# Kernel optimization log

Measured on AMD Instinct MI355X. Metric: run time of the kernel, lower is better.

The kernel has to match this reference:

```python
import jax, jax.numpy as jnp
import numpy as np
import math

B, S, HID = 1, 2048, 2048
H, KVH, HD = 16, 4, 128
LEVEL = 256


def _rope_tables(seq_len, dim, dtype=jnp.float32):
    inv_freq = 1.0 / (10000.0 ** (np.arange(0, dim, 2, dtype=np.float32) / dim))
    ang = np.arange(seq_len, dtype=np.float32)[:, None] * inv_freq[None, :]  # [S, HD/2]
    emb = np.concatenate([ang, ang], axis=-1)  # [S, HD]
    return jnp.asarray(np.cos(emb), dtype)[None], jnp.asarray(np.sin(emb), dtype)[None]


def setup_inputs() -> dict:
    key = jax.random.key(0)
    ks = jax.random.split(key, 6)
    hidden_states = jax.random.normal(ks[0], (B, S, HID), jnp.float32)
    w_std = 1.0 / math.sqrt(HID)
    Wq = jax.random.normal(ks[1], (H * HD, HID), jnp.float32) * w_std
    Wk = jax.random.normal(ks[2], (KVH * HD, HID), jnp.float32) * w_std
    Wv = jax.random.normal(ks[3], (KVH * HD, HID), jnp.float32) * w_std
    Wo = jax.random.normal(ks[4], (HID, H * HD), jnp.float32) * w_std
    cos, sin = _rope_tables(S, HD)
    # additive causal mask [1,1,S,S]
    tri = jnp.tril(jnp.ones((S, S), jnp.bool_))
    attention_mask = jnp.where(tri, 0.0, -1e9).astype(jnp.float32)[None, None]
    return {
        "hidden_states": hidden_states,
        "Wq": Wq, "Wk": Wk, "Wv": Wv, "Wo": Wo,
        "s_q": jnp.full((1,), 0.05, jnp.float32),
        "s_k": jnp.full((1,), 0.05, jnp.float32),
        "s_v": jnp.full((1,), 0.05, jnp.float32),
        "s_attn": jnp.full((1,), 0.004, jnp.float32),
        "s_out": jnp.full((1,), 0.02, jnp.float32),
        "cos": cos, "sin": sin,
        "attention_mask": attention_mask,
    }


def _lsq(x, s, level, sym):
    # LSQ fake-quant: learned per-tensor step s, STE round, LSQ grad-scale on s.
    if sym:
        qn, qp = -level // 2, level // 2 - 1
    else:
        qn, qp = 0, level - 1
    g = 1.0 / math.sqrt(x.size * qp)          # LSQ gradient scale (static)
    s = jnp.abs(s)
    s_eff = s * g + jax.lax.stop_gradient(s - s * g)  # fwd = s, bwd grad *= g
    v = jnp.clip(x / s_eff, qn, qp)
    q = v + jax.lax.stop_gradient(jnp.round(v) - v)   # STE round
    return q * s_eff


def _rotate_half(x):
    x1, x2 = jnp.split(x, 2, axis=-1)
    return jnp.concatenate([-x2, x1], axis=-1)


def _attn_fwd(hidden_states, Wq, Wk, Wv, Wo, s_q, s_k, s_v, s_attn, s_out,
              cos, sin, attention_mask):
    b, s_len, _ = hidden_states.shape
    # projections -> [B, heads, S, HD]
    q = (hidden_states @ Wq.T).reshape(b, s_len, H, HD).transpose(0, 2, 1, 3)
    q = _lsq(q, s_q, LEVEL, sym=True)
    k = (hidden_states @ Wk.T).reshape(b, s_len, KVH, HD).transpose(0, 2, 1, 3)
    k = _lsq(k, s_k, LEVEL, sym=True)
    v = (hidden_states @ Wv.T).reshape(b, s_len, KVH, HD).transpose(0, 2, 1, 3)
    v = _lsq(v, s_v, LEVEL, sym=True)
    # RoPE (after quant, matching source order)
    c, si = cos[:, None], sin[:, None]  # [B,1,S,HD]
    q = q * c + _rotate_half(q) * si
    k = k * c + _rotate_half(k) * si
    # GQA repeat
    groups = H // KVH
    k = jnp.repeat(k, groups, axis=1)
    v = jnp.repeat(v, groups, axis=1)
    scores = jnp.einsum("bhqd,bhkd->bhqk", q, k) / math.sqrt(HD)
    scores = scores + attention_mask[:, :, :, :s_len]
    attn = jax.nn.softmax(scores.astype(jnp.float32), axis=-1).astype(q.dtype)
    attn = _lsq(attn, s_attn, LEVEL, sym=False)
    out = jnp.einsum("bhqk,bhkd->bhqd", attn, v)
    out = _lsq(out, s_out, LEVEL, sym=False)
    out = out.transpose(0, 2, 1, 3).reshape(b, s_len, H * HD)
    out = out @ Wo.T
    return out, attn


def reference(hidden_states, Wq, Wk, Wv, Wo, s_q, s_k, s_v, s_attn, s_out,
              cos, sin, attention_mask):
    return _attn_fwd(hidden_states, Wq, Wk, Wv, Wo, s_q, s_k, s_v, s_attn,
                     s_out, cos, sin, attention_mask)
```

## Files before the change

kernel.cpp:

```cpp
#include <hip/hip_runtime.h>
#include <math.h>

#define S_LEN 2048
#define HID_DIM 2048
#define NH 16
#define NKVH 4
#define HD 128
#define QD (NH*HD)
#define KD (NKVH*HD)
#define NQKV 3072

typedef _Float16 half8_t __attribute__((ext_vector_type(8)));
typedef _Float16 half4_t __attribute__((ext_vector_type(4)));
typedef float f32x4 __attribute__((ext_vector_type(4)));

#define BM 128
#define BN 128
#define BK 32

typedef const __attribute__((address_space(1))) char gas_char;
typedef __attribute__((address_space(3))) char las_char;
#define GL16(gp, lp) __builtin_amdgcn_global_load_lds((gas_char*)(gp), (las_char*)(lp), 16, 0, 0)

template<int LA, int LB, bool AF32, bool PSM>
__global__ __launch_bounds__(256)
void gemm_f16(const void* __restrict__ Ap, const _Float16* __restrict__ Alo,
              int lda, long long strA,
              const _Float16* __restrict__ Bhi, const _Float16* __restrict__ Blo,
              int ldb, long long strB, int divB,
              void* __restrict__ Cp, int ldc, long long strC,
              int K, float scale_c, const float* sc1, const float* sc2,
              const float* preAp,
              int qmode, const float* q1, const float* q2, const float* q3,
              int causal, int triK, float* __restrict__ pml)
{
    int bz = blockIdx.z;
    int m0 = blockIdx.y * BM, n0 = blockIdx.x * BN;
    if (causal && n0 > m0 + (BM - 1)) return;
    int Keff = K;
    if (triK && (m0 + BM) < Keff) Keff = m0 + BM;

    const _Float16* Ahi = AF32 ? nullptr : (const _Float16*)Ap + bz * strA;
    const _Float16* AloP = (LA == 2) ? Alo + bz * strA : nullptr;
    const float* Af = AF32 ? (const float*)Ap + bz * strA : nullptr;
    const _Float16* BhiP = Bhi + (long long)(bz / divB) * strB;
    const _Float16* BloP = (LB == 2) ? Blo + (long long)(bz / divB) * strB : nullptr;
    float* Cf = (float*)Cp + bz * strC;
    _Float16* Ch = (_Float16*)Cp + bz * strC;

    float preA = 1.f;
    if (AF32) preA = 1.f / fabsf(preAp[0]);

    __shared__ _Float16 lds[(LA + LB) * 4096];
    _Float16* As0 = lds;
    _Float16* As1 = lds + 4096;
    _Float16* Bs0 = lds + LA * 4096;
    _Float16* Bs1 = lds + (LA + 1) * 4096;

    int t = threadIdx.x;
    int srow = t >> 2;
    int gsw = (srow >> 1) & 3;
    int gc = ((t & 3) ^ gsw) * 8;
    int w = t >> 6, lane = t & 63;
    int wm = (w >> 1) * 64, wn = (w & 1) * 64;
    int lr = lane & 15, lg = lane >> 4;
    int fco = ((lg ^ ((lr >> 1) & 3))) * 8;

    f32x4 acc[4][4];
    #pragma unroll
    for (int i = 0; i < 4; ++i)
        #pragma unroll
        for (int j = 0; j < 4; ++j)
            acc[i][j] = (f32x4){0.f, 0.f, 0.f, 0.f};

    for (int k0 = 0; k0 < Keff; k0 += BK) {
        f32x4 aF[2][2];
        if constexpr (AF32) {
            #pragma unroll
            for (int rep = 0; rep < 2; ++rep) {
                long long ai = (long long)(m0 + rep * 64 + srow) * lda + k0 + gc;
                aF[rep][0] = *(const f32x4*)&Af[ai];
                aF[rep][1] = *(const f32x4*)&Af[ai + 4];
            }
        }
        __syncthreads();
        #pragma unroll
        for (int rep = 0; rep < 2; ++rep) {
            int row = rep * 64 + srow;
            int lo = rep * 2048 + t * 8;
            if constexpr (!AF32) {
                long long ai = (long long)(m0 + row) * lda + k0 + gc;
                GL16(Ahi + ai, As0 + lo);
                if constexpr (LA == 2) GL16(AloP + ai, As1 + lo);
            }
            long long bi = (long long)(n0 + row) * ldb + k0 + gc;
            GL16(BhiP + bi, Bs0 + lo);
            if constexpr (LB == 2) GL16(BloP + bi, Bs1 + lo);
        }
        if constexpr (AF32) {
            #pragma unroll
            for (int rep = 0; rep < 2; ++rep) {
                half8_t h;
                #pragma unroll
                for (int e = 0; e < 4; ++e) {
                    h[e]     = (_Float16)(aF[rep][0][e] * preA);
                    h[e + 4] = (_Float16)(aF[rep][1][e] * preA);
                }
                *(half8_t*)&As0[rep * 2048 + t * 8] = h;
            }
        }
        __syncthreads();

        half8_t a0[4], b0[4];
        #pragma unroll
        for (int i = 0; i < 4; ++i) a0[i] = *(const half8_t*)&As0[(wm + i*16 + lr) * 32 + fco];
        #pragma unroll
        for (int j = 0; j < 4; ++j) b0[j] = *(const half8_t*)&Bs0[(wn + j*16 + lr) * 32 + fco];
        #pragma unroll
        for (int i = 0; i < 4; ++i)
            #pragma unroll
            for (int j = 0; j < 4; ++j)
                acc[i][j] = __builtin_amdgcn_mfma_f32_16x16x32_f16(a0[i], b0[j], acc[i][j], 0, 0, 0);
        if constexpr (LB == 2) {
            half8_t b1[4];
            #pragma unroll
            for (int j = 0; j < 4; ++j) b1[j] = *(const half8_t*)&Bs1[(wn + j*16 + lr) * 32 + fco];
            #pragma unroll
            for (int i = 0; i < 4; ++i)
                #pragma unroll
                for (int j = 0; j < 4; ++j)
                    acc[i][j] = __builtin_amdgcn_mfma_f32_16x16x32_f16(a0[i], b1[j], acc[i][j], 0, 0, 0);
        }
        if constexpr (LA == 2) {
            half8_t a1[4];
            #pragma unroll
            for (int i = 0; i < 4; ++i) a1[i] = *(const half8_t*)&As1[(wm + i*16 + lr) * 32 + fco];
            #pragma unroll
            for (int i = 0; i < 4; ++i)
                #pragma unroll
                for (int j = 0; j < 4; ++j)
                    acc[i][j] = __builtin_amdgcn_mfma_f32_16x16x32_f16(a1[i], b0[j], acc[i][j], 0, 0, 0);
        }
    }

    float se = scale_c;
    if (sc1) se *= fabsf(sc1[0]);
    if (sc2) se *= fabsf(sc2[0]);
    float sv = 1.f;
    if (qmode == 3) {
        const float* sp = (n0 < 2048) ? q1 : ((n0 < 2560) ? q2 : q3);
        sv = fabsf(sp[0]);
        qmode = 1;
    } else if (qmode) {
        sv = fabsf(q1[0]);
    }

    #pragma unroll
    for (int i = 0; i < 4; ++i)
        #pragma unroll
        for (int j = 0; j < 4; ++j)
            #pragma unroll
            for (int r = 0; r < 4; ++r) {
                long long row = m0 + wm + i * 16 + lg * 4 + r;
                long long col = n0 + wn + j * 16 + lr;
                float v = acc[i][j][r] * se;
                if (qmode == 0) {
                    Cf[row * (long long)ldc + col] = v;
                } else if (qmode == 1) {
                    float u = rintf(fminf(fmaxf(v / sv, -128.f), 127.f));
                    Ch[row * (long long)ldc + col] = (_Float16)u;
                } else {
                    float u = rintf(fminf(fmaxf(v / sv, 0.f), 255.f));
                    Ch[row * (long long)ldc + col] = (_Float16)u;
                }
            }

    if constexpr (PSM) {
        int cb64 = (n0 + wn) >> 6;
        #pragma unroll
        for (int i = 0; i < 4; ++i)
            #pragma unroll
            for (int r = 0; r < 4; ++r) {
                int row = m0 + wm + i * 16 + lg * 4 + r;
                float vv[4];
                float mloc = -INFINITY;
                #pragma unroll
                for (int j = 0; j < 4; ++j) {
                    int col = n0 + wn + j * 16 + lr;
                    float v = acc[i][j][r] * se;
                    vv[j] = (col <= row) ? v : -INFINITY;
                    mloc = fmaxf(mloc, vv[j]);
                }
                #pragma unroll
                for (int o = 1; o < 16; o <<= 1) mloc = fmaxf(mloc, __shfl_xor(mloc, o));
                float sloc = 0.f;
                #pragma unroll
                for (int j = 0; j < 4; ++j) sloc += expf(vv[j] - mloc);
                #pragma unroll
                for (int o = 1; o < 16; o <<= 1) sloc += __shfl_xor(sloc, o);
                if (lr == 0) {
                    long long idx = (((long long)bz * S_LEN + row) * 32 + cb64) * 2;
                    pml[idx] = mloc;
                    pml[idx + 1] = sloc;
                }
            }
    }
}

__global__ __launch_bounds__(256)
void reduce_ml(const float* __restrict__ pml, float* __restrict__ fml)
{
    int id = blockIdx.x * 256 + threadIdx.x;
    int r = id & (S_LEN - 1);
    int nb = (r >> 6) + 1;
    float m = -INFINITY, l = 0.f;
    const float* p = pml + (long long)id * 64;
    for (int cb = 0; cb < nb; ++cb) {
        float mp = p[cb * 2], lp = p[cb * 2 + 1];
        float mn = fmaxf(m, mp);
        l = l * expf(m - mn) + lp * expf(mp - mn);
        m = mn;
    }
    fml[id * 2] = m;
    fml[id * 2 + 1] = l;
}

__global__ __launch_bounds__(256)
void fused_pv(float* __restrict__ attn, const _Float16* __restrict__ vT,
              const float* __restrict__ fml, _Float16* __restrict__ ao,
              const float* s_at_p, const float* s_v_p, const float* s_out_p)
{
    int rb = blockIdx.x;
    int h = blockIdx.y;
    int m0 = rb * 64;
    float* S = attn + (long long)h * S_LEN * S_LEN;
    const _Float16* V = vT + (long long)(h >> 2) * HD * S_LEN;

    float sa = fabsf(s_at_p[0]);
    float seo = sa * fabsf(s_v_p[0]) / fabsf(s_out_p[0]);

    __shared__ _Float16 Bs[128 * 32];
    __shared__ float ml[64][2];

    int t = threadIdx.x;
    int w = t >> 6, lane = t & 63;
    int lr = lane & 15, lg = lane >> 4;
    int wr0 = m0 + w * 16;
    int row = wr0 + lr;

    if (t < 64) {
        ml[t][0] = fml[((long long)h * S_LEN + m0 + t) * 2];
        ml[t][1] = fml[((long long)h * S_LEN + m0 + t) * 2 + 1];
    }
    __syncthreads();
    float mrow = ml[w * 16 + lr][0];
    float lrow = ml[w * 16 + lr][1];

    int srow = t >> 2;
    int gsw = (srow >> 1) & 3;
    int gc = ((t & 3) ^ gsw) * 8;
    int fco = ((lg ^ ((lr >> 1) & 3))) * 8;

    f32x4 acc[8];
    #pragma unroll
    for (int j = 0; j < 8; ++j) acc[j] = (f32x4){0.f, 0.f, 0.f, 0.f};

    int kmax = m0 + 64;
    for (int k0 = 0; k0 < kmax; k0 += 32) {
        __syncthreads();
        #pragma unroll
        for (int rep = 0; rep < 2; ++rep)
            GL16(&V[(long long)(rep * 64 + srow) * S_LEN + k0 + gc], &Bs[rep * 2048 + t * 8]);

        int c0 = k0 + lg * 8;
        long long sbase = (long long)row * S_LEN + c0;
        f32x4 s1 = *(const f32x4*)&S[sbase];
        f32x4 s2 = *(const f32x4*)&S[sbase + 4];
        half8_t af;
        f32x4 o1, o2;
        #pragma unroll
        for (int e = 0; e < 8; ++e) {
            float sv_ = (e < 4) ? s1[e] : s2[e - 4];
            float u = 0.f;
            if (c0 + e <= row) {
                float p = expf(sv_ - mrow) / lrow;
                u = rintf(fminf(fmaxf(p / sa, 0.f), 255.f));
            }
            af[e] = (_Float16)u;
            if (e < 4) o1[e] = u * sa; else o2[e - 4] = u * sa;
        }
        *(f32x4*)&S[sbase] = o1;
        *(f32x4*)&S[sbase + 4] = o2;

        __syncthreads();
        if (k0 <= wr0 + 15) {
            half8_t bf[8];
            #pragma unroll
            for (int j = 0; j < 8; ++j)
                bf[j] = *(const half8_t*)&Bs[(j * 16 + lr) * 32 + fco];
            #pragma unroll
            for (int j = 0; j < 8; ++j)
                acc[j] = __builtin_amdgcn_mfma_f32_16x16x32_f16(af, bf[j], acc[j], 0, 0, 0);
        }
    }

    {
        int rr = t >> 2, l4 = (t & 3) * 4;
        f32x4 z = (f32x4){0.f, 0.f, 0.f, 0.f};
        for (int cc = kmax + l4; cc < S_LEN; cc += 16)
            *(f32x4*)&S[(long long)(m0 + rr) * S_LEN + cc] = z;
    }

    #pragma unroll
    for (int j = 0; j < 8; ++j)
        #pragma unroll
        for (int r = 0; r < 4; ++r) {
            int orow = wr0 + lg * 4 + r;
            int d = j * 16 + lr;
            float u = rintf(fminf(fmaxf(acc[j][r] * seo, 0.f), 255.f));
            ao[(long long)orow * QD + h * HD + d] = (_Float16)u;
        }
}

__global__ void split_f16(const float* __restrict__ in, _Float16* __restrict__ hi,
                          _Float16* __restrict__ lo, int n4)
{
    int i = blockIdx.x * 256 + threadIdx.x;
    if (i >= n4) return;
    f32x4 v = ((const f32x4*)in)[i];
    half4_t h, l;
    #pragma unroll
    for (int e = 0; e < 4; ++e) {
        h[e] = (_Float16)v[e];
        l[e] = (_Float16)(v[e] - (float)h[e]);
    }
    ((half4_t*)hi)[i] = h;
    ((half4_t*)lo)[i] = l;
}

__global__ void rope_f16(const _Float16* __restrict__ codes, int ldc_, int colOff,
                         const float* __restrict__ cosT,
                         const float* __restrict__ sinT,
                         _Float16* __restrict__ ohi, _Float16* __restrict__ olo, int nh)
{
    long long idx = (long long)blockIdx.x * 256 + threadIdx.x;
    int d = idx & (HD - 1);
    long long tt = idx >> 7;
    int h = (int)(tt % nh);
    int s = (int)(tt / nh);
    long long base = (long long)s * ldc_ + colOff + h * HD;
    float x = (float)codes[base + d];
    float other = (d < 64) ? -(float)codes[base + d + 64] : (float)codes[base + d - 64];
    float o = x * cosT[s * HD + d] + other * sinT[s * HD + d];
    _Float16 hf = (_Float16)o;
    long long oi = ((long long)h * S_LEN + s) * HD + d;
    ohi[oi] = hf;
    olo[oi] = (_Float16)(o - (float)hf);
}

__global__ __launch_bounds__(256)
void transpose_vf16(const _Float16* __restrict__ in, _Float16* __restrict__ outp)
{
    __shared__ _Float16 tile[64][72];
    int s0 = blockIdx.x * 64, d0 = blockIdx.y * 64, h = blockIdx.z;
    int t = threadIdx.x;
    int rr = t >> 4, cc = (t & 15) * 4;
    #pragma unroll
    for (int r = 0; r < 4; ++r) {
        half4_t v = *(const half4_t*)&in[(long long)(s0 + rr + 16*r) * NQKV + 2560 + h * HD + d0 + cc];
        *(half4_t*)&tile[rr + 16*r][cc] = v;
    }
    __syncthreads();
    #pragma unroll
    for (int r = 0; r < 4; ++r) {
        int dr = rr + 16 * r;
        half4_t o = { tile[cc+0][dr], tile[cc+1][dr], tile[cc+2][dr], tile[cc+3][dr] };
        *(half4_t*)&outp[((long long)h * HD + d0 + dr) * S_LEN + s0 + cc] = o;
    }
}

extern "C" void kernel_launch(void* const* d_in, const int* in_sizes, int n_in,
                              void* d_out, int out_size, void* d_ws, size_t ws_size,
                              hipStream_t stream)
{
    const float* hs    = (const float*)d_in[0];
    const float* Wq    = (const float*)d_in[1];
    const float* Wk    = (const float*)d_in[2];
    const float* Wv    = (const float*)d_in[3];
    const float* Wo    = (const float*)d_in[4];
    const float* s_q   = (const float*)d_in[5];
    const float* s_k   = (const float*)d_in[6];
    const float* s_v   = (const float*)d_in[7];
    const float* s_at  = (const float*)d_in[8];
    const float* s_out = (const float*)d_in[9];
    const float* cosT  = (const float*)d_in[10];
    const float* sinT  = (const float*)d_in[11];

    float* out  = (float*)d_out;
    float* attn = out + (long long)S_LEN * HID_DIM;

    const long long M1 = 1LL * 1024 * 1024;
    const long long M4 = 4LL * M1;
    const long long M6 = 6LL * M1;

    _Float16* wsh   = (_Float16*)d_ws;
    _Float16* qr_hi = wsh;
    _Float16* qr_lo = qr_hi + M4;
    _Float16* kr_hi = qr_lo + M4;
    _Float16* kr_lo = kr_hi + M1;
    _Float16* vT    = kr_lo + M1;
    _Float16* ao    = vT + M1;
    _Float16* Wo_hi = ao + M4;
    _Float16* Wo_lo = Wo_hi + M4;

    _Float16* sc      = (_Float16*)attn;
    _Float16* hs_hi   = sc;
    _Float16* hs_lo   = hs_hi + M4;
    _Float16* Whi     = hs_lo + M4;
    _Float16* Wlo     = Whi + M6;
    _Float16* qkvcode = Wlo + M6;

    float* pml = out;
    float* fml = out + 2LL * 1024 * 1024;

    dim3 blk(256);
    const float iscale = 0.08838834764831845f;

    split_f16<<<4096, blk, 0, stream>>>(hs, hs_hi, hs_lo, 1024*1024);
    split_f16<<<4096, blk, 0, stream>>>(Wq, Whi, Wlo, 1024*1024);
    split_f16<<<1024, blk, 0, stream>>>(Wk, Whi + 2048LL*2048, Wlo + 2048LL*2048, 256*1024);
    split_f16<<<1024, blk, 0, stream>>>(Wv, Whi + 2560LL*2048, Wlo + 2560LL*2048, 256*1024);
    split_f16<<<4096, blk, 0, stream>>>(Wo, Wo_hi, Wo_lo, 1024*1024);

    gemm_f16<2,2,false,false><<<dim3(NQKV/BN, S_LEN/BM, 1), blk, 0, stream>>>(
        hs_hi, hs_lo, HID_DIM, 0, Whi, Wlo, HID_DIM, 0, 1,
        qkvcode, NQKV, 0, HID_DIM, 1.f, nullptr, nullptr, nullptr,
        3, s_q, s_k, s_v, 0, 0, nullptr);

    rope_f16<<<(NH*S_LEN*HD)/256, blk, 0, stream>>>(qkvcode, NQKV, 0, cosT, sinT, qr_hi, qr_lo, NH);
    rope_f16<<<(NKVH*S_LEN*HD)/256, blk, 0, stream>>>(qkvcode, NQKV, 2048, cosT, sinT, kr_hi, kr_lo, NKVH);
    transpose_vf16<<<dim3(S_LEN/64, HD/64, NKVH), blk, 0, stream>>>(qkvcode, vT);

    gemm_f16<2,2,false,true><<<dim3(S_LEN/BN, S_LEN/BM, NH), blk, 0, stream>>>(
        qr_hi, qr_lo, HD, (long long)S_LEN*HD,
        kr_hi, kr_lo, HD, (long long)S_LEN*HD, NH/NKVH,
        attn, S_LEN, (long long)S_LEN*S_LEN,
        HD, iscale, s_q, s_k, nullptr, 0, nullptr, nullptr, nullptr, 1, 0, pml);

    reduce_ml<<<(NH*S_LEN)/256, blk, 0, stream>>>(pml, fml);

    fused_pv<<<dim3(S_LEN/64, NH), blk, 0, stream>>>(
        attn, vT, fml, ao, s_at, s_v, s_out);

    gemm_f16<1,2,false,false><<<dim3(HID_DIM/BN, S_LEN/BM, 1), blk, 0, stream>>>(
        ao, nullptr, QD, 0, Wo_hi, Wo_lo, QD, 0, 1,
        out, HID_DIM, 0, QD, 1.f, s_out, nullptr, nullptr,
        0, nullptr, nullptr, nullptr, 0, 0, nullptr);
}
```

Before: 551.4 us.

## Split fused PV into finalize pass plus split-K atomic GEMM

Replaces the fused softmax-quantize-PV kernel with three steps. A row-wise finalize kernel normalizes and quantizes the attention probabilities in place. A split-K GEMM then reads the fp32 attention matrix, scaled to integer codes by 1/s_attn, and accumulates P·V into a zeroed fp32 buffer with atomics, with the K range chunked into 512-wide pieces and trimmed at the causal boundary. A separate kernel quantizes the accumulator into f16 codes. The intent is more parallelism across K and better load balance for the causal rows, at the cost of an extra full pass over the attention matrix, a memset, atomic traffic and a larger workspace.

```diff
diff --git a/kernel.cpp b/kernel.cpp
--- a/kernel.cpp
+++ b/kernel.cpp
@@ -17,12 +17,13 @@
 #define BM 128
 #define BN 128
 #define BK 32
+#define KCHUNK 512
 
 typedef const __attribute__((address_space(1))) char gas_char;
 typedef __attribute__((address_space(3))) char las_char;
 #define GL16(gp, lp) __builtin_amdgcn_global_load_lds((gas_char*)(gp), (las_char*)(lp), 16, 0, 0)
 
-template<int LA, int LB, bool AF32, bool PSM>
+template<int LA, int LB, bool AF32, bool PSM, bool ATOMK>
 __global__ __launch_bounds__(256)
 void gemm_f16(const void* __restrict__ Ap, const _Float16* __restrict__ Alo,
               int lda, long long strA,
@@ -35,10 +36,18 @@
               int causal, int triK, float* __restrict__ pml)
 {
     int bz = blockIdx.z;
-    int m0 = blockIdx.y * BM, n0 = blockIdx.x * BN;
+    int m0 = blockIdx.y * BM;
+    int n0 = ATOMK ? 0 : blockIdx.x * BN;
     if (causal && n0 > m0 + (BM - 1)) return;
     int Keff = K;
     if (triK && (m0 + BM) < Keff) Keff = m0 + BM;
+
+    int kbeg = 0, kend = Keff;
+    if constexpr (ATOMK) {
+        kbeg = blockIdx.x * KCHUNK;
+        kend = min(Keff, kbeg + KCHUNK);
+        if (kbeg >= kend) return;
+    }
 
     const _Float16* Ahi = AF32 ? nullptr : (const _Float16*)Ap + bz * strA;
     const _Float16* AloP = (LA == 2) ? Alo + bz * strA : nullptr;
@@ -73,7 +82,7 @@
         for (int j = 0; j < 4; ++j)
             acc[i][j] = (f32x4){0.f, 0.f, 0.f, 0.f};
 
-    for (int k0 = 0; k0 < Keff; k0 += BK) {
+    for (int k0 = kbeg; k0 < kend; k0 += BK) {
         f32x4 aF[2][2];
         if constexpr (AF32) {
             #pragma unroll
@@ -141,6 +150,20 @@
                 for (int j = 0; j < 4; ++j)
                     acc[i][j] = __builtin_amdgcn_mfma_f32_16x16x32_f16(a1[i], b0[j], acc[i][j], 0, 0, 0);
         }
+    }
+
+    if constexpr (ATOMK) {
+        #pragma unroll
+        for (int i = 0; i < 4; ++i)
+            #pragma unroll
+            for (int j = 0; j < 4; ++j)
+                #pragma unroll
+                for (int r = 0; r < 4; ++r) {
+                    long long row = m0 + wm + i * 16 + lg * 4 + r;
+                    long long col = n0 + wn + j * 16 + lr;
+                    atomicAdd(&Cf[row * (long long)ldc + col], acc[i][j][r]);
+                }
+        return;
     }
 
     float se = scale_c;
@@ -226,100 +249,45 @@
 }
 
 __global__ __launch_bounds__(256)
-void fused_pv(float* __restrict__ attn, const _Float16* __restrict__ vT,
-              const float* __restrict__ fml, _Float16* __restrict__ ao,
-              const float* s_at_p, const float* s_v_p, const float* s_out_p)
-{
-    int rb = blockIdx.x;
-    int h = blockIdx.y;
-    int m0 = rb * 64;
-    float* S = attn + (long long)h * S_LEN * S_LEN;
-    const _Float16* V = vT + (long long)(h >> 2) * HD * S_LEN;
-
+void finalize_quant(float* __restrict__ attn, const float* __restrict__ fml,
+                    const float* __restrict__ s_at_p)
+{
+    int row = blockIdx.x;
+    int q = row & (S_LEN - 1);
+    float* p = attn + (long long)row * S_LEN;
+    float m = fml[row * 2];
+    float l = fml[row * 2 + 1];
     float sa = fabsf(s_at_p[0]);
-    float seo = sa * fabsf(s_v_p[0]) / fabsf(s_out_p[0]);
-
-    __shared__ _Float16 Bs[128 * 32];
-    __shared__ float ml[64][2];
-
     int t = threadIdx.x;
-    int w = t >> 6, lane = t & 63;
-    int lr = lane & 15, lg = lane >> 4;
-    int wr0 = m0 + w * 16;
-    int row = wr0 + lr;
-
-    if (t < 64) {
-        ml[t][0] = fml[((long long)h * S_LEN + m0 + t) * 2];
-        ml[t][1] = fml[((long long)h * S_LEN + m0 + t) * 2 + 1];
-    }
-    __syncthreads();
-    float mrow = ml[w * 16 + lr][0];
-    float lrow = ml[w * 16 + lr][1];
-
-    int srow = t >> 2;
-    int gsw = (srow >> 1) & 3;
-    int gc = ((t & 3) ^ gsw) * 8;
-    int fco = ((lg ^ ((lr >> 1) & 3))) * 8;
-
-    f32x4 acc[8];
-    #pragma unroll
-    for (int j = 0; j < 8; ++j) acc[j] = (f32x4){0.f, 0.f, 0.f, 0.f};
-
-    int kmax = m0 + 64;
-    for (int k0 = 0; k0 < kmax; k0 += 32) {
-        __syncthreads();
-        #pragma unroll
-        for (int rep = 0; rep < 2; ++rep)
-            GL16(&V[(long long)(rep * 64 + srow) * S_LEN + k0 + gc], &Bs[rep * 2048 + t * 8]);
-
-        int c0 = k0 + lg * 8;
-        long long sbase = (long long)row * S_LEN + c0;
-        f32x4 s1 = *(const f32x4*)&S[sbase];
-        f32x4 s2 = *(const f32x4*)&S[sbase + 4];
-        half8_t af;
-        f32x4 o1, o2;
-        #pragma unroll
-        for (int e = 0; e < 8; ++e) {
-            float sv_ = (e < 4) ? s1[e] : s2[e - 4];
+    #pragma unroll
+    for (int c = t * 4; c < S_LEN; c += 1024) {
+        f32x4 v = *(const f32x4*)&p[c];
+        f32x4 o;
+        #pragma unroll
+        for (int e = 0; e < 4; ++e) {
             float u = 0.f;
-            if (c0 + e <= row) {
-                float p = expf(sv_ - mrow) / lrow;
-                u = rintf(fminf(fmaxf(p / sa, 0.f), 255.f));
-            }
-            af[e] = (_Float16)u;
-            if (e < 4) o1[e] = u * sa; else o2[e - 4] = u * sa;
-        }
-        *(f32x4*)&S[sbase] = o1;
-        *(f32x4*)&S[sbase + 4] = o2;
-
-        __syncthreads();
-        if (k0 <= wr0 + 15) {
-            half8_t bf[8];
-            #pragma unroll
-            for (int j = 0; j < 8; ++j)
-                bf[j] = *(const half8_t*)&Bs[(j * 16 + lr) * 32 + fco];
-            #pragma unroll
-            for (int j = 0; j < 8; ++j)
-                acc[j] = __builtin_amdgcn_mfma_f32_16x16x32_f16(af, bf[j], acc[j], 0, 0, 0);
-        }
-    }
-
-    {
-        int rr = t >> 2, l4 = (t & 3) * 4;
-        f32x4 z = (f32x4){0.f, 0.f, 0.f, 0.f};
-        for (int cc = kmax + l4; cc < S_LEN; cc += 16)
-            *(f32x4*)&S[(long long)(m0 + rr) * S_LEN + cc] = z;
-    }
-
-    #pragma unroll
-    for (int j = 0; j < 8; ++j)
-        #pragma unroll
-        for (int r = 0; r < 4; ++r) {
-            int orow = wr0 + lg * 4 + r;
-            int d = j * 16 + lr;
-            float u = rintf(fminf(fmaxf(acc[j][r] * seo, 0.f), 255.f));
-            ao[(long long)orow * QD + h * HD + d] = (_Float16)u;
-        }
+            if (c + e <= q) {
+                float pr = expf(v[e] - m) / l;
+                u = rintf(fminf(fmaxf(pr / sa, 0.f), 255.f));
+            }
+            o[e] = u * sa;
+        }
+        *(f32x4*)&p[c] = o;
+    }
+}
+
+__global__ __launch_bounds__(256)
+void quant_ao(const float* __restrict__ acc, _Float16* __restrict__ ao,
+              const float* sa_p, const float* sv_p, const float* so_p)
+{
+    int i = blockIdx.x * 256 + threadIdx.x;
+    float seo = fabsf(sa_p[0]) * fabsf(sv_p[0]) / fabsf(so_p[0]);
+    f32x4 v = ((const f32x4*)acc)[i];
+    half4_t o;
+    #pragma unroll
+    for (int e = 0; e < 4; ++e)
+        o[e] = (_Float16)rintf(fminf(fmaxf(v[e] * seo, 0.f), 255.f));
+    ((half4_t*)ao)[i] = o;
 }
 
 __global__ void split_f16(const float* __restrict__ in, _Float16* __restrict__ hi,
@@ -412,6 +380,7 @@
     _Float16* ao    = vT + M1;
     _Float16* Wo_hi = ao + M4;
     _Float16* Wo_lo = Wo_hi + M4;
+    float*    ao_acc = (float*)(Wo_lo + M4);
 
     _Float16* sc      = (_Float16*)attn;
     _Float16* hs_hi   = sc;
@@ -432,7 +401,7 @@
     split_f16<<<1024, blk, 0, stream>>>(Wv, Whi + 2560LL*2048, Wlo + 2560LL*2048, 256*1024);
     split_f16<<<4096, blk, 0, stream>>>(Wo, Wo_hi, Wo_lo, 1024*1024);
 
-    gemm_f16<2,2,false,false><<<dim3(NQKV/BN, S_LEN/BM, 1), blk, 0, stream>>>(
+    gemm_f16<2,2,false,false,false><<<dim3(NQKV/BN, S_LEN/BM, 1), blk, 0, stream>>>(
         hs_hi, hs_lo, HID_DIM, 0, Whi, Wlo, HID_DIM, 0, 1,
         qkvcode, NQKV, 0, HID_DIM, 1.f, nullptr, nullptr, nullptr,
         3, s_q, s_k, s_v, 0, 0, nullptr);
@@ -441,7 +410,7 @@
     rope_f16<<<(NKVH*S_LEN*HD)/256, blk, 0, stream>>>(qkvcode, NQKV, 2048, cosT, sinT, kr_hi, kr_lo, NKVH);
     transpose_vf16<<<dim3(S_LEN/64, HD/64, NKVH), blk, 0, stream>>>(qkvcode, vT);
 
-    gemm_f16<2,2,false,true><<<dim3(S_LEN/BN, S_LEN/BM, NH), blk, 0, stream>>>(
+    gemm_f16<2,2,false,true,false><<<dim3(S_LEN/BN, S_LEN/BM, NH), blk, 0, stream>>>(
         qr_hi, qr_lo, HD, (long long)S_LEN*HD,
         kr_hi, kr_lo, HD, (long long)S_LEN*HD, NH/NKVH,
         attn, S_LEN, (long long)S_LEN*S_LEN,
@@ -449,10 +418,17 @@
 
     reduce_ml<<<(NH*S_LEN)/256, blk, 0, stream>>>(pml, fml);
 
-    fused_pv<<<dim3(S_LEN/64, NH), blk, 0, stream>>>(
-        attn, vT, fml, ao, s_at, s_v, s_out);
-
-    gemm_f16<1,2,false,false><<<dim3(HID_DIM/BN, S_LEN/BM, 1), blk, 0, stream>>>(
+    finalize_quant<<<NH*S_LEN, blk, 0, stream>>>(attn, fml, s_at);
+
+    hipMemsetAsync(ao_acc, 0, (size_t)S_LEN * QD * sizeof(float), stream);
+    gemm_f16<1,1,true,false,true><<<dim3(S_LEN/KCHUNK, S_LEN/BM, NH), blk, 0, stream>>>(
+        attn, nullptr, S_LEN, (long long)S_LEN*S_LEN,
+        vT, nullptr, S_LEN, (long long)HD*S_LEN, NH/NKVH,
+        ao_acc, QD, HD,
+        S_LEN, 1.f, nullptr, nullptr, s_at, 0, nullptr, nullptr, nullptr, 0, 1, nullptr);
+    quant_ao<<<(S_LEN*QD)/1024, blk, 0, stream>>>(ao_acc, ao, s_at, s_v, s_out);
+
+    gemm_f16<1,2,false,false,false><<<dim3(HID_DIM/BN, S_LEN/BM, 1), blk, 0, stream>>>(
         ao, nullptr, QD, 0, Wo_hi, Wo_lo, QD, 0, 1,
         out, HID_DIM, 0, QD, 1.f, s_out, nullptr, nullptr,
         0, nullptr, nullptr, nullptr, 0, 0, nullptr);
```

New measurement: 557.7 us. Within noise of the previous version (+1.1%).
